# Performance work log

Measured on AMD Instinct MI355X. Metric: run time of the kernel, lower is better.

## Reference

```python
import jax, jax.numpy as jnp
import numpy as np
from itertools import combinations_with_replacement

KSIZE = 13  # 1 + 6*int(start_scale) with start_scale=2.0 (fixed at init)


def gaussian_kernel3d(scale):
    # torch: sigma = max(0.1, min(sigma, 10)); kernel detached (requires_grad=False)
    sigma = jnp.clip(jax.lax.stop_gradient(scale), 0.1, 10.0)
    k1 = jnp.arange(KSIZE, dtype=jnp.float32) - KSIZE // 2
    k1 = jnp.exp(-(k1 ** 2) / (2.0 * sigma ** 2))
    k3 = jnp.einsum('i,j,k->ijk', k1, k1, k1)
    return k3 / k3.sum()


def blur3d(vol, kernel):
    # replicate ('edge') padding then VALID conv, matching padding_mode='replicate'
    p = KSIZE // 2
    vp = jnp.pad(vol, ((0, 0), (0, 0), (p, p), (p, p), (p, p)), mode='edge')
    w = kernel[None, None]  # [O=1, I=1, kD, kH, kW]
    return jax.lax.conv_general_dilated(
        vp, w, window_strides=(1, 1, 1), padding='VALID',
        dimension_numbers=('NCDHW', 'OIDHW', 'NCDHW'))


def tgrad(f, axis):
    # torch.gradient: central diff interior, one-sided first-order at edges
    n = f.shape[axis]
    sl = lambda a, b: jax.lax.slice_in_dim(f, a, b, axis=axis)
    interior = (sl(2, n) - sl(0, n - 2)) * 0.5
    first = sl(1, 2) - sl(0, 1)
    last = sl(n - 1, n) - sl(n - 2, n - 1)
    return jnp.concatenate([first, interior, last], axis=axis)


def setup_inputs() -> dict:
    key = jax.random.key(0)
    kx, k1, k2, k3, k4 = jax.random.split(key, 5)
    B, D, H, W = 2, 128, 128, 128
    x = jax.random.normal(kx, (B, 1, D, H, W), dtype=jnp.float32)
    scale = jnp.asarray(2.0, dtype=jnp.float32)
    # Linear(7,10) and Linear(10,1), torch layout [out, in]
    lim1 = 1.0 / np.sqrt(7.0)
    lim2 = 1.0 / np.sqrt(10.0)
    W1 = jax.random.uniform(k1, (10, 7), jnp.float32, -lim1, lim1)
    b1 = jax.random.uniform(k2, (10,), jnp.float32, -lim1, lim1)
    W2 = jax.random.uniform(k3, (1, 10), jnp.float32, -lim2, lim2)
    b2 = jax.random.uniform(k4, (1,), jnp.float32, -lim2, lim2)
    return {'x': x, 'scale': scale, 'W1': W1, 'b1': b1, 'W2': W2, 'b2': b2}


def reference(x, scale, W1, b1, W2, b2):
    B = x.shape[0]
    D, H, W = x.shape[2], x.shape[3], x.shape[4]
    smoothed = blur3d(x, gaussian_kernel3d(scale))  # [B,1,D,H,W]
    axes = [2, 3, 4]
    g = [tgrad(smoothed, a) for a in axes]
    H_elems = [tgrad(g[a0 - 2], a1) for a0, a1 in combinations_with_replacement(axes, 2)]
    h = jnp.stack(H_elems)                      # [6,B,1,D,H,W]
    h = jnp.moveaxis(h, 0, -1)                  # [B,1,D,H,W,6]
    h = h.reshape(B, D * H * W, 6)              # flatten dims 1..4 (C=1)
    scale_col = jnp.broadcast_to(scale, (B, D * H * W, 1))
    feat = jnp.concatenate([h, scale_col], axis=2)  # [B,N,7]
    hid = jax.nn.relu(feat @ W1.T + b1)             # [B,N,10]
    out = jax.nn.sigmoid(hid @ W2.T + b2)           # [B,N,1]
    out = out.reshape(B, D, H, W, 1)
    return jnp.transpose(out, (0, 4, 1, 2, 3))      # [B,1,D,H,W]
```

## Files before the change

### kernel.cpp

```cpp
#include <hip/hip_runtime.h>
#include <math.h>

#define NVOX (2 * 128 * 128 * 128)
#define KS 13
#define KR 6
#define LROWS 44

__device__ __forceinline__ float4 LD4(const float* p) {
    return *reinterpret_cast<const float4*>(p);
}

__device__ __forceinline__ void make_weights(float scale, float* wv) {
    float sig = fminf(fmaxf(scale, 0.1f), 10.0f);
    float inv2s2 = -1.0f / (2.0f * sig * sig);
    float sum = 0.f;
#pragma unroll
    for (int t = 0; t < KS; ++t) {
        float d = (float)(t - KR);
        wv[t] = __expf(d * d * inv2s2);
        sum += wv[t];
    }
    float r = 1.0f / sum;
#pragma unroll
    for (int t = 0; t < KS; ++t) wv[t] *= r;
}

__global__ __launch_bounds__(256) void wh_blur_kernel(const float* __restrict__ in,
                                                      float* __restrict__ out,
                                                      const float* __restrict__ scale_p) {
    __shared__ float T[LROWS * 128];
    const int slice = blockIdx.x >> 2;
    const int h0 = (blockIdx.x & 3) << 5;
    const float* sp = in + (slice << 14);
    float* op = out + (slice << 14);

    float wv[KS];
    make_weights(scale_p[0], wv);

    for (int it = 0; it < 6; ++it) {
        int g = threadIdx.x + (it << 8);
        if (g < LROWS * 32) {
            int w0 = (g & 31) << 2;
            int lr = g >> 5;
            int r = h0 - 6 + lr;
            r = r < 0 ? 0 : (r > 127 ? 127 : r);
            const float* rp = sp + (r << 7);

            float F[20];
            if (w0 >= 8 && w0 <= 116) {
                float4 q0 = LD4(rp + w0 - 8), q1 = LD4(rp + w0 - 4), q2 = LD4(rp + w0),
                       q3 = LD4(rp + w0 + 4), q4 = LD4(rp + w0 + 8);
                F[0] = q0.x; F[1] = q0.y; F[2] = q0.z; F[3] = q0.w;
                F[4] = q1.x; F[5] = q1.y; F[6] = q1.z; F[7] = q1.w;
                F[8] = q2.x; F[9] = q2.y; F[10] = q2.z; F[11] = q2.w;
                F[12] = q3.x; F[13] = q3.y; F[14] = q3.z; F[15] = q3.w;
                F[16] = q4.x; F[17] = q4.y; F[18] = q4.z; F[19] = q4.w;
            } else {
#pragma unroll
                for (int i = 0; i < 16; ++i) {
                    int ww = w0 - 6 + i;
                    ww = ww < 0 ? 0 : (ww > 127 ? 127 : ww);
                    F[i + 2] = rp[ww];
                }
            }
            float a0 = 0.f, a1 = 0.f, a2 = 0.f, a3 = 0.f;
#pragma unroll
            for (int t = 0; t < KS; ++t) {
                float wt = wv[t];
                a0 = fmaf(wt, F[2 + t], a0);
                a1 = fmaf(wt, F[3 + t], a1);
                a2 = fmaf(wt, F[4 + t], a2);
                a3 = fmaf(wt, F[5 + t], a3);
            }
            *reinterpret_cast<float4*>(&T[(lr << 7) + w0]) = make_float4(a0, a1, a2, a3);
        }
    }
    __syncthreads();

    {
        const int w0 = (threadIdx.x & 31) << 2;
        const int r0 = (threadIdx.x >> 5) << 2;

        float4 win[KS];
#pragma unroll
        for (int t = 0; t < KS; ++t) win[t] = LD4(&T[((r0 + t) << 7) + w0]);
#pragma unroll
        for (int s = 0; s < 4; ++s) {
            float4 acc = make_float4(0.f, 0.f, 0.f, 0.f);
#pragma unroll
            for (int t = 0; t < KS; ++t) {
                float4 v = win[(s + t) % KS];
                float wt = wv[t];
                acc.x = fmaf(wt, v.x, acc.x);
                acc.y = fmaf(wt, v.y, acc.y);
                acc.z = fmaf(wt, v.z, acc.z);
                acc.w = fmaf(wt, v.w, acc.w);
            }
            *reinterpret_cast<float4*>(op + ((h0 + r0 + s) << 7) + w0) = acc;
            int nl = r0 + s + 13;
            nl = nl > LROWS - 1 ? LROWS - 1 : nl;
            win[s % KS] = LD4(&T[(nl << 7) + w0]);
        }
    }
}

__global__ __launch_bounds__(256) void dblur_kernel(const float* __restrict__ in,
                                                    float* __restrict__ out,
                                                    const float* __restrict__ scale_p) {
    const int t0 = blockIdx.x * 256 + threadIdx.x;
    const int w0 = (t0 & 31) << 2;
    const int h  = (t0 >> 5) & 127;
    const int d0 = ((t0 >> 12) & 15) << 3;
    const int b  = t0 >> 16;
    const int base = (b << 21) | (h << 7) | w0;

    float wv[KS];
    make_weights(scale_p[0], wv);

    float4 win[KS];
#pragma unroll
    for (int t = 0; t < KS; ++t) {
        int r = d0 - 6 + t;
        r = r < 0 ? 0 : (r > 127 ? 127 : r);
        win[t] = LD4(in + base + (r << 14));
    }
#pragma unroll
    for (int s = 0; s < 8; ++s) {
        float4 acc = make_float4(0.f, 0.f, 0.f, 0.f);
#pragma unroll
        for (int t = 0; t < KS; ++t) {
            float4 v = win[(s + t) % KS];
            float wt = wv[t];
            acc.x = fmaf(wt, v.x, acc.x);
            acc.y = fmaf(wt, v.y, acc.y);
            acc.z = fmaf(wt, v.z, acc.z);
            acc.w = fmaf(wt, v.w, acc.w);
        }
        *reinterpret_cast<float4*>(out + base + ((d0 + s) << 14)) = acc;
        int rn = d0 + s + 7;
        rn = rn > 127 ? 127 : rn;
        win[s % KS] = LD4(in + base + (rn << 14));
    }
}

__device__ __forceinline__ void lohi(int c, int& lo, int& hi, float& s) {
    lo = c > 0 ? c - 1 : 0;
    hi = c < 127 ? c + 1 : 127;
    s = 1.0f / (float)(hi - lo);
}

__device__ __forceinline__ int CH(int v) {
    return v < 0 ? 0 : (v > 127 ? 127 : v);
}

__global__ __launch_bounds__(256) void hess_mlp_kernel(const float* __restrict__ S,
                                const float* __restrict__ scale_p,
                                const float* __restrict__ W1, const float* __restrict__ b1,
                                const float* __restrict__ W2, const float* __restrict__ b2,
                                float* __restrict__ out) {
    const int t = blockIdx.x * 256 + threadIdx.x;
    const int l = t & 31;
    const int w0 = l << 2;
    const int hb = ((t >> 5) & 31) << 2;
    const int d = (t >> 10) & 127;
    const int b = t >> 17;
    const int lane = threadIdx.x & 63;
    const bool l0 = (l == 0), l31 = (l == 31);

    int ld, hd; float sd; lohi(d, ld, hd, sd);
    int ti, tj; float s_hd, s_ld;
    lohi(hd, ti, tj, s_hd); lohi(ld, ti, tj, s_ld);
    const bool d_top = (d == 127), d_bot = (d == 0);
    const int dp2 = d > 125 ? 127 : d + 2;
    const int dm2 = d < 2 ? 0 : d - 2;

    float sw[4], s_hw[4], s_lw[4];
#pragma unroll
    for (int j = 0; j < 4; ++j) {
        int lw, hw; lohi(w0 + j, lw, hw, sw[j]);
        lohi(hw, ti, tj, s_hw[j]); lohi(lw, ti, tj, s_lw[j]);
    }

    const float scale = scale_p[0];
    float b1e[10];
#pragma unroll
    for (int u = 0; u < 10; ++u) b1e[u] = fmaf(scale, W1[u * 7 + 6], b1[u]);

    const float* base = S + (b << 21) + w0;
    auto RP = [&](int dd, int hh) { return base + (dd << 14) + (hh << 7); };
    float* obase = out + (b << 21) + (d << 14) + w0;

    float4 nd0 = LD4(RP(d, CH(hb - 2))), nd1 = LD4(RP(d, CH(hb - 1))),
           nd2 = LD4(RP(d, hb)),        nd3 = LD4(RP(d, hb + 1)),
           nd4 = LD4(RP(d, CH(hb + 2)));
    float4 pm0 = LD4(RP(ld, CH(hb - 1))), pm1 = LD4(RP(ld, hb)), pm2 = LD4(RP(ld, hb + 1));
    float4 pp0 = LD4(RP(hd, CH(hb - 1))), pp1 = LD4(RP(hd, hb)), pp2 = LD4(RP(hd, hb + 1));

#pragma unroll
    for (int s = 0; s < 4; ++s) {
        const int h = hb + s;
        const float4 qp = LD4(RP(dp2, h));
        const float4 qm = LD4(RP(dm2, h));

        int lh, hh; float sh; lohi(h, lh, hh, sh);
        float s_hh, s_lh; lohi(hh, ti, tj, s_hh); lohi(lh, ti, tj, s_lh);
        const bool h_top = (h == 127), h_bot = (h == 0);

        float c_lz = __shfl(nd2.z, lane - 1), c_lw = __shfl(nd2.w, lane - 1);
        float c_rx = __shfl(nd2.x, lane + 1), c_ry = __shfl(nd2.y, lane + 1);
        float r1_lw = __shfl(nd1.w, lane - 1), r1_rx = __shfl(nd1.x, lane + 1);
        float r3_lw = __shfl(nd3.w, lane - 1), r3_rx = __shfl(nd3.x, lane + 1);
        float pmlw = __shfl(pm1.w, lane - 1), pmrx = __shfl(pm1.x, lane + 1);
        float pplw = __shfl(pp1.w, lane - 1), pprx = __shfl(pp1.x, lane + 1);

        const float va[4]  = {nd2.x, nd2.y, nd2.z, nd2.w};
        const float n0a[4] = {nd0.x, nd0.y, nd0.z, nd0.w};
        const float n1a[4] = {nd1.x, nd1.y, nd1.z, nd1.w};
        const float n3a[4] = {nd3.x, nd3.y, nd3.z, nd3.w};
        const float n4a[4] = {nd4.x, nd4.y, nd4.z, nd4.w};
        const float pm0a[4] = {pm0.x, pm0.y, pm0.z, pm0.w};
        const float pm1a[4] = {pm1.x, pm1.y, pm1.z, pm1.w};
        const float pm2a[4] = {pm2.x, pm2.y, pm2.z, pm2.w};
        const float pp0a[4] = {pp0.x, pp0.y, pp0.z, pp0.w};
        const float pp1a[4] = {pp1.x, pp1.y, pp1.z, pp1.w};
        const float pp2a[4] = {pp2.x, pp2.y, pp2.z, pp2.w};
        const float qpa[4] = {qp.x, qp.y, qp.z, qp.w};
        const float qma[4] = {qm.x, qm.y, qm.z, qm.w};

        const float c_m1[4] = {l0 ? va[0] : c_lw, va[0], va[1], va[2]};
        const float c_p1[4] = {va[1], va[2], va[3], l31 ? va[3] : c_rx};
        const float c_m2[4] = {l0 ? va[0] : c_lz, l0 ? va[0] : c_lw, va[0], va[1]};
        const float c_p2[4] = {va[2], va[3], l31 ? va[3] : c_rx, l31 ? va[3] : c_ry};
        const float r1m[4] = {l0 ? n1a[0] : r1_lw, n1a[0], n1a[1], n1a[2]};
        const float r1p[4] = {n1a[1], n1a[2], n1a[3], l31 ? n1a[3] : r1_rx};
        const float r3m[4] = {l0 ? n3a[0] : r3_lw, n3a[0], n3a[1], n3a[2]};
        const float r3p[4] = {n3a[1], n3a[2], n3a[3], l31 ? n3a[3] : r3_rx};
        const float pmm[4] = {l0 ? pm1a[0] : pmlw, pm1a[0], pm1a[1], pm1a[2]};
        const float pmp[4] = {pm1a[1], pm1a[2], pm1a[3], l31 ? pm1a[3] : pmrx};
        const float ppm[4] = {l0 ? pp1a[0] : pplw, pp1a[0], pp1a[1], pp1a[2]};
        const float ppp[4] = {pp1a[1], pp1a[2], pp1a[3], l31 ? pp1a[3] : pprx};

        float ov[4];
#pragma unroll
        for (int j = 0; j < 4; ++j) {
            const float fDD = sd * (s_hd * (qpa[j] - (d_top ? pm1a[j] : va[j]))
                                  - s_ld * ((d_bot ? pp1a[j] : va[j]) - qma[j]));
            const float fHH = sh * (s_hh * (n4a[j] - (h_top ? n1a[j] : va[j]))
                                  - s_lh * ((h_bot ? n3a[j] : va[j]) - n0a[j]));
            const float fDH = sd * sh * ((pp2a[j] - pp0a[j]) - (pm2a[j] - pm0a[j]));
            const float fHW = sh * sw[j] * ((r3p[j] - r3m[j]) - (r1p[j] - r1m[j]));
            const float fDW = sd * sw[j] * ((ppp[j] - ppm[j]) - (pmp[j] - pmm[j]));
            const float Aw = (j == 3 && l31) ? c_m1[j] : va[j];
            const float Bw = (j == 0 && l0) ? c_p1[j] : va[j];
            const float fWW = sw[j] * (s_hw[j] * (c_p2[j] - Aw) - s_lw[j] * (Bw - c_m2[j]));

            const float ft[6] = {fDD, fDH, fDW, fHH, fHW, fWW};
            float o = b2[0];
#pragma unroll
            for (int u = 0; u < 10; ++u) {
                float a = b1e[u];
#pragma unroll
                for (int k = 0; k < 6; ++k) a = fmaf(ft[k], W1[u * 7 + k], a);
                a = fmaxf(a, 0.f);
                o = fmaf(a, W2[u], o);
            }
            float e = __expf(-o);
            ov[j] = __builtin_amdgcn_rcpf(1.0f + e);
        }
        *reinterpret_cast<float4*>(obase + (h << 7)) = make_float4(ov[0], ov[1], ov[2], ov[3]);

        nd0 = nd1; nd1 = nd2; nd2 = nd3; nd3 = nd4;
        nd4 = LD4(RP(d, CH(h + 3)));
        pm0 = pm1; pm1 = pm2; pm2 = LD4(RP(ld, CH(h + 2)));
        pp0 = pp1; pp1 = pp2; pp2 = LD4(RP(hd, CH(h + 2)));
    }
}

extern "C" void kernel_launch(void* const* d_in, const int* in_sizes, int n_in,
                              void* d_out, int out_size, void* d_ws, size_t ws_size,
                              hipStream_t stream) {
    const float* x     = (const float*)d_in[0];
    const float* scale = (const float*)d_in[1];
    const float* W1    = (const float*)d_in[2];
    const float* b1    = (const float*)d_in[3];
    const float* W2    = (const float*)d_in[4];
    const float* b2    = (const float*)d_in[5];
    float* out = (float*)d_out;

    float* ws0 = (float*)d_ws;
    float* ws1 = ws0 + NVOX;

    wh_blur_kernel<<<2 * 128 * 4, 256, 0, stream>>>(x, ws1, scale);
    dblur_kernel<<<NVOX / 32 / 256, 256, 0, stream>>>(ws1, ws0, scale);
    hess_mlp_kernel<<<NVOX / 16 / 256, 256, 0, stream>>>(ws0, scale, W1, b1, W2, b2, out);
}
```

Before: 48.34 us.

## Swizzle block order across kernels and pack MLP into float2 vector math

Each of the three kernels now remaps blockIdx with an interleave of stride eight, changing which slices and tiles run concurrently, presumably to spread work across XCDs and improve L2 locality. The per-voxel MLP in the hessian kernel now processes two voxels at a time with float2 ext-vector arithmetic, so the compiler can emit packed FP32 FMA and max instructions. b2 is also hoisted into a register. Register pressure may rise and the remapped order could hurt cache reuse.

After: 56.46 us. 16.8% more time.

```diff
diff --git a/kernel.cpp b/kernel.cpp
--- a/kernel.cpp
+++ b/kernel.cpp
@@ -6,6 +6,8 @@
 #define KR 6
 #define LROWS 44
 
+typedef float f2 __attribute__((ext_vector_type(2)));
+
 __device__ __forceinline__ float4 LD4(const float* p) {
     return *reinterpret_cast<const float4*>(p);
 }
@@ -29,8 +31,10 @@
                                                       float* __restrict__ out,
                                                       const float* __restrict__ scale_p) {
     __shared__ float T[LROWS * 128];
-    const int slice = blockIdx.x >> 2;
-    const int h0 = (blockIdx.x & 3) << 5;
+    const int i = blockIdx.x;
+    const int wid = ((i & 7) << 7) | (i >> 3);
+    const int slice = wid >> 2;
+    const int h0 = (wid & 3) << 5;
     const float* sp = in + (slice << 14);
     float* op = out + (slice << 14);
 
@@ -57,10 +61,10 @@
                 F[16] = q4.x; F[17] = q4.y; F[18] = q4.z; F[19] = q4.w;
             } else {
 #pragma unroll
-                for (int i = 0; i < 16; ++i) {
-                    int ww = w0 - 6 + i;
+                for (int i2 = 0; i2 < 16; ++i2) {
+                    int ww = w0 - 6 + i2;
                     ww = ww < 0 ? 0 : (ww > 127 ? 127 : ww);
-                    F[i + 2] = rp[ww];
+                    F[i2 + 2] = rp[ww];
                 }
             }
             float a0 = 0.f, a1 = 0.f, a2 = 0.f, a3 = 0.f;
@@ -107,7 +111,9 @@
 __global__ __launch_bounds__(256) void dblur_kernel(const float* __restrict__ in,
                                                     float* __restrict__ out,
                                                     const float* __restrict__ scale_p) {
-    const int t0 = blockIdx.x * 256 + threadIdx.x;
+    const int i = blockIdx.x;
+    const int wid = ((i & 7) << 6) | (i >> 3);
+    const int t0 = wid * 256 + threadIdx.x;
     const int w0 = (t0 & 31) << 2;
     const int h  = (t0 >> 5) & 127;
     const int d0 = ((t0 >> 12) & 15) << 3;
@@ -158,7 +164,9 @@
                                 const float* __restrict__ W1, const float* __restrict__ b1,
                                 const float* __restrict__ W2, const float* __restrict__ b2,
                                 float* __restrict__ out) {
-    const int t = blockIdx.x * 256 + threadIdx.x;
+    const int i = blockIdx.x;
+    const int wid = ((i & 7) << 7) | (i >> 3);
+    const int t = wid * 256 + threadIdx.x;
     const int l = t & 31;
     const int w0 = l << 2;
     const int hb = ((t >> 5) & 31) << 2;
@@ -182,6 +190,7 @@
     }
 
     const float scale = scale_p[0];
+    const float b2s = b2[0];
     float b1e[10];
 #pragma unroll
     for (int u = 0; u < 10; ++u) b1e[u] = fmaf(scale, W1[u * 7 + 6], b1[u]);
@@ -242,30 +251,40 @@
 
         float ov[4];
 #pragma unroll
-        for (int j = 0; j < 4; ++j) {
-            const float fDD = sd * (s_hd * (qpa[j] - (d_top ? pm1a[j] : va[j]))
-                                  - s_ld * ((d_bot ? pp1a[j] : va[j]) - qma[j]));
-            const float fHH = sh * (s_hh * (n4a[j] - (h_top ? n1a[j] : va[j]))
-                                  - s_lh * ((h_bot ? n3a[j] : va[j]) - n0a[j]));
-            const float fDH = sd * sh * ((pp2a[j] - pp0a[j]) - (pm2a[j] - pm0a[j]));
-            const float fHW = sh * sw[j] * ((r3p[j] - r3m[j]) - (r1p[j] - r1m[j]));
-            const float fDW = sd * sw[j] * ((ppp[j] - ppm[j]) - (pmp[j] - pmm[j]));
-            const float Aw = (j == 3 && l31) ? c_m1[j] : va[j];
-            const float Bw = (j == 0 && l0) ? c_p1[j] : va[j];
-            const float fWW = sw[j] * (s_hw[j] * (c_p2[j] - Aw) - s_lw[j] * (Bw - c_m2[j]));
-
-            const float ft[6] = {fDD, fDH, fDW, fHH, fHW, fWW};
-            float o = b2[0];
+        for (int p = 0; p < 2; ++p) {
+            f2 F0, F1, F2v, F3, F4, F5;
+#pragma unroll
+            for (int jj = 0; jj < 2; ++jj) {
+                const int j = p * 2 + jj;
+                const float fDD = sd * (s_hd * (qpa[j] - (d_top ? pm1a[j] : va[j]))
+                                      - s_ld * ((d_bot ? pp1a[j] : va[j]) - qma[j]));
+                const float fHH = sh * (s_hh * (n4a[j] - (h_top ? n1a[j] : va[j]))
+                                      - s_lh * ((h_bot ? n3a[j] : va[j]) - n0a[j]));
+                const float fDH = sd * sh * ((pp2a[j] - pp0a[j]) - (pm2a[j] - pm0a[j]));
+                const float fHW = sh * sw[j] * ((r3p[j] - r3m[j]) - (r1p[j] - r1m[j]));
+                const float fDW = sd * sw[j] * ((ppp[j] - ppm[j]) - (pmp[j] - pmm[j]));
+                const float Aw = (j == 3 && l31) ? c_m1[j] : va[j];
+                const float Bw = (j == 0 && l0) ? c_p1[j] : va[j];
+                const float fWW = sw[j] * (s_hw[j] * (c_p2[j] - Aw) - s_lw[j] * (Bw - c_m2[j]));
+                F0[jj] = fDD; F1[jj] = fDH; F2v[jj] = fDW;
+                F3[jj] = fHH; F4[jj] = fHW; F5[jj] = fWW;
+            }
+            f2 o = (f2){b2s, b2s};
 #pragma unroll
             for (int u = 0; u < 10; ++u) {
-                float a = b1e[u];
-#pragma unroll
-                for (int k = 0; k < 6; ++k) a = fmaf(ft[k], W1[u * 7 + k], a);
-                a = fmaxf(a, 0.f);
-                o = fmaf(a, W2[u], o);
-            }
-            float e = __expf(-o);
-            ov[j] = __builtin_amdgcn_rcpf(1.0f + e);
+                f2 a = (f2){b1e[u], b1e[u]};
+                a += F0 * W1[u * 7 + 0];
+                a += F1 * W1[u * 7 + 1];
+                a += F2v * W1[u * 7 + 2];
+                a += F3 * W1[u * 7 + 3];
+                a += F4 * W1[u * 7 + 4];
+                a += F5 * W1[u * 7 + 5];
+                a = __builtin_elementwise_max(a, (f2){0.f, 0.f});
+                o += a * W2[u];
+            }
+            float e0 = __expf(-o.x), e1 = __expf(-o.y);
+            ov[p * 2]     = __builtin_amdgcn_rcpf(1.0f + e0);
+            ov[p * 2 + 1] = __builtin_amdgcn_rcpf(1.0f + e1);
         }
         *reinterpret_cast<float4*>(obase + (h << 7)) = make_float4(ov[0], ov[1], ov[2], ov[3]);
 
```
